# Optimization experiments

Hardware: AMD Instinct MI355X
Metric: run time of the kernel (lower is better)

The kernel has to match this reference:

```python
import jax, jax.numpy as jnp
import numpy as np

N_NODES = 100000
N_EDGES = 1600000
N_GRAPHS = 2048
DIM_IN, DIM_H, DIM_FC, DIM_OUT = 128, 128, 256, 8


def _glorot(key, shape):
    fan_in, fan_out = shape[0], shape[1]
    lim = float(np.sqrt(6.0 / (fan_in + fan_out)))
    return jax.random.uniform(key, shape, jnp.float32, -lim, lim)


def setup_inputs() -> dict:
    key = jax.random.key(0)
    ks = jax.random.split(key, 16)
    x = jax.random.normal(ks[0], (N_NODES, DIM_IN), jnp.float32)
    edge_index = jax.random.randint(ks[1], (2, N_EDGES), 0, N_NODES, jnp.int64)
    batch = jnp.sort(jax.random.randint(ks[2], (N_NODES,), 0, N_GRAPHS, jnp.int64))
    inp = {"x": x, "edge_index": edge_index, "batch": batch}
    # GraphConv layers: W_rel [in,out], W_root [in,out], b [out]
    dims = [(DIM_IN, DIM_H), (DIM_H, DIM_H), (DIM_H, DIM_H), (DIM_H, DIM_H)]
    for i, (di, do) in enumerate(dims, start=1):
        inp[f"W{i}_rel"] = _glorot(ks[2 + 3 * i], (di, do))
        inp[f"W{i}_root"] = _glorot(ks[3 + 3 * i], (di, do))
        inp[f"b{i}"] = jnp.zeros((do,), jnp.float32)
    inp["fc_w"] = _glorot(ks[3], (DIM_H, DIM_FC))
    inp["fc_b"] = jnp.zeros((DIM_FC,), jnp.float32)
    inp["reg_w"] = _glorot(ks[4], (DIM_FC, DIM_OUT))
    inp["reg_b"] = jnp.zeros((DIM_OUT,), jnp.float32)
    return inp


def _graph_conv(x, src, dst, w_rel, w_root, b):
    # PyG GraphConv (aggr='add'): out_i = W_rel @ sum_{j->i} x_j + W_root @ x_i + b
    agg = jax.ops.segment_sum(x[src], dst, num_segments=N_NODES)  # [N, d_in]
    return agg @ w_rel + x @ w_root + b


def reference(x, edge_index, batch,
              W1_rel, W1_root, b1, W2_rel, W2_root, b2,
              W3_rel, W3_root, b3, W4_rel, W4_root, b4,
              fc_w, fc_b, reg_w, reg_b):
    src, dst = edge_index[0], edge_index[1]
    h = jax.nn.relu(_graph_conv(x, src, dst, W1_rel, W1_root, b1))
    h = jax.nn.relu(_graph_conv(h, src, dst, W2_rel, W2_root, b2))
    h = jax.nn.relu(_graph_conv(h, src, dst, W3_rel, W3_root, b3))
    h = jax.nn.relu(_graph_conv(h, src, dst, W4_rel, W4_root, b4))
    # global_mean_pool over graphs
    sums = jax.ops.segment_sum(h, batch, num_segments=N_GRAPHS)  # [G, d]
    cnt = jax.ops.segment_sum(jnp.ones((h.shape[0],), h.dtype), batch,
                              num_segments=N_GRAPHS)
    pooled = sums / jnp.maximum(cnt, 1.0)[:, None]
    # dropout is identity at inference
    hfc = pooled @ fc_w + fc_b
    return hfc @ reg_w + reg_b  # [G, dim_out]
```

## Files before the change

### kernel.cpp

```cpp
#include <hip/hip_runtime.h>

#define N_NODES 100000
#define N_EDGES 1600000
#define N_GRAPHS 2048
#define DIM 128

#define NBUK 196
#define BUKSH 9
#define NCH 256
#define EPB 6250
#define NMAT (NBUK * NCH)

typedef short short8v __attribute__((ext_vector_type(8)));
typedef float float4v __attribute__((ext_vector_type(4)));

__device__ __forceinline__ unsigned short f2bf(float f) {
  union { float f; unsigned u; } x; x.f = f;
  unsigned r = x.u + 0x7fffu + ((x.u >> 16) & 1u);
  return (unsigned short)(r >> 16);
}
__device__ __forceinline__ float bfhi2f(unsigned bits) {
  union { unsigned u; float f; } x; x.u = bits; return x.f;
}
__device__ __forceinline__ void accum8(float* p, uint4 v) {
  p[0] += bfhi2f(v.x << 16); p[1] += bfhi2f(v.x & 0xffff0000u);
  p[2] += bfhi2f(v.y << 16); p[3] += bfhi2f(v.y & 0xffff0000u);
  p[4] += bfhi2f(v.z << 16); p[5] += bfhi2f(v.z & 0xffff0000u);
  p[6] += bfhi2f(v.w << 16); p[7] += bfhi2f(v.w & 0xffff0000u);
}

__global__ __launch_bounds__(256) void k_bcount(const int* __restrict__ dst, int* __restrict__ cntmat) {
  __shared__ int cnt[NBUK];
  int b = blockIdx.x, t = threadIdx.x;
  if (t < NBUK) cnt[t] = 0;
  __syncthreads();
  int e0 = b * EPB;
  for (int j = t; j < EPB; j += 256) atomicAdd(&cnt[dst[e0 + j] >> BUKSH], 1);
  __syncthreads();
  if (t < NBUK) cntmat[t * NCH + b] = cnt[t];
}

__global__ __launch_bounds__(256) void k_scan1g(const int* __restrict__ in, int n,
                                                int* __restrict__ tmp, int* __restrict__ bsum) {
  __shared__ int sh[256];
  int b = blockIdx.x, t = threadIdx.x;
  int base = b * 1024 + t * 4;
  int v[4], s = 0;
#pragma unroll
  for (int i = 0; i < 4; i++) { v[i] = (base + i < n) ? in[base + i] : 0; s += v[i]; }
  sh[t] = s;
  __syncthreads();
  for (int off = 1; off < 256; off <<= 1) {
    int x = (t >= off) ? sh[t - off] : 0;
    __syncthreads();
    sh[t] += x;
    __syncthreads();
  }
  int run = sh[t] - s;
#pragma unroll
  for (int i = 0; i < 4; i++) { run += v[i]; if (base + i < n) tmp[base + i] = run; }
  if (t == 255) bsum[b] = sh[255];
}

__global__ void k_scan2g(int* __restrict__ bsum, int nb) {
  __shared__ int sh[128];
  int t = threadIdx.x;
  int v = (t < nb) ? bsum[t] : 0;
  sh[t] = v;
  __syncthreads();
  for (int off = 1; off < 128; off <<= 1) {
    int x = (t >= off) ? sh[t - off] : 0;
    __syncthreads();
    sh[t] += x;
    __syncthreads();
  }
  if (t < nb) bsum[t] = sh[t] - v;
}

__global__ __launch_bounds__(256) void k_exc(const int* __restrict__ tmp, const int* __restrict__ bsum,
                                             const int* __restrict__ in, int n, int* __restrict__ outExc) {
  int i = blockIdx.x * 256 + threadIdx.x;
  if (i < n) outExc[i] = tmp[i] + bsum[i >> 10] - in[i];
}

__global__ __launch_bounds__(256) void k_bscatter(const int* __restrict__ src, const int* __restrict__ dst,
                                                  const int* __restrict__ base, int2* __restrict__ epk) {
  __shared__ int cur[NBUK];
  int b = blockIdx.x, t = threadIdx.x;
  if (t < NBUK) cur[t] = base[t * NCH + b];
  __syncthreads();
  int e0 = b * EPB;
  for (int j = t; j < EPB; j += 256) {
    int s = src[e0 + j], d = dst[e0 + j];
    int pos = atomicAdd(&cur[d >> BUKSH], 1);
    epk[pos] = make_int2(s, d);
  }
}

__global__ __launch_bounds__(256) void k_bfinish(const int2* __restrict__ epk, const int* __restrict__ base,
                                                 int* __restrict__ rowptr, int* __restrict__ col) {
  __shared__ int a[512];
  __shared__ int sh[256];
  int k = blockIdx.x, t = threadIdx.x;
  int bstart = base[k * NCH];
  int bend = (k + 1 < NBUK) ? base[(k + 1) * NCH] : N_EDGES;
  a[t] = 0; a[t + 256] = 0;
  __syncthreads();
  for (int i = bstart + t; i < bend; i += 256) atomicAdd(&a[epk[i].y - (k << BUKSH)], 1);
  __syncthreads();
  int c0 = a[2 * t], c1 = a[2 * t + 1];
  int s = c0 + c1;
  sh[t] = s;
  __syncthreads();
  for (int off = 1; off < 256; off <<= 1) {
    int x = (t >= off) ? sh[t - off] : 0;
    __syncthreads();
    sh[t] += x;
    __syncthreads();
  }
  int excl = sh[t] - s;
  int st0 = bstart + excl;
  int st1 = st0 + c0;
  int g0 = (k << BUKSH) + 2 * t, g1 = g0 + 1;
  if (g0 < N_NODES) rowptr[g0] = st0;
  if (g1 < N_NODES) rowptr[g1] = st1;
  if (k == NBUK - 1 && t == 0) rowptr[N_NODES] = N_EDGES;
  __syncthreads();
  a[2 * t] = st0; a[2 * t + 1] = st1;
  __syncthreads();
  for (int i = bstart + t; i < bend; i += 256) {
    int2 e = epk[i];
    int pos = atomicAdd(&a[e.y - (k << BUKSH)], 1);
    col[pos] = e.x;
  }
}

__global__ __launch_bounds__(256) void k_gptr(const int* __restrict__ batch, int* __restrict__ gptr) {
  int i = blockIdx.x * 256 + threadIdx.x;
  if (i >= N_NODES) return;
  int b = batch[i];
  int a = (i == 0) ? -1 : batch[i - 1];
  for (int g = a + 1; g <= b; g++) gptr[g] = i;
  if (i == N_NODES - 1) {
    for (int g = b + 1; g <= N_GRAPHS; g++) gptr[g] = N_NODES;
  }
}

__global__ __launch_bounds__(256) void k_cvtx(const float* __restrict__ x, unsigned short* __restrict__ h) {
  int i = blockIdx.x * 256 + threadIdx.x;
  if (i < N_NODES * DIM / 4) {
    float4 v = ((const float4*)x)[i];
    unsigned lo = (unsigned)f2bf(v.x) | ((unsigned)f2bf(v.y) << 16);
    unsigned hi = (unsigned)f2bf(v.z) | ((unsigned)f2bf(v.w) << 16);
    ((uint2*)h)[i] = make_uint2(lo, hi);
  }
}

__global__ __launch_bounds__(256) void k_cvtw(const float* w0, const float* w1, const float* w2, const float* w3,
                                              const float* w4, const float* w5, const float* w6, const float* w7,
                                              unsigned short* __restrict__ wbF) {
  int i = blockIdx.x * 256 + threadIdx.x;
  if (i < 4 * 8 * 8 * 64 * 8) {
    int j = i & 7, l = (i >> 3) & 63, c = (i >> 9) & 7, kc = (i >> 12) & 7, layer = i >> 15;
    int m = layer * 2 + (kc >> 2);
    const float* w;
    switch (m) {
      case 0: w = w0; break; case 1: w = w1; break; case 2: w = w2; break; case 3: w = w3; break;
      case 4: w = w4; break; case 5: w = w5; break; case 6: w = w6; break; default: w = w7; break;
    }
    int kin = (kc & 3) * 32 + ((l >> 4) * 8) + j;
    int n = c * 16 + (l & 15);
    wbF[i] = f2bf(w[kin * 128 + n]);
  }
}

__global__ __launch_bounds__(256, 8) void k_fused(const int* __restrict__ rowptr,
                                                  const int* __restrict__ col,
                                                  const unsigned short* __restrict__ hIn,
                                                  const unsigned short* __restrict__ wbF,
                                                  const float* __restrict__ bias,
                                                  unsigned short* __restrict__ hOut) {
  __shared__ uint4 As[1024];
  const int t = threadIdx.x;
  const int wave = t >> 6, lane = t & 63;
  const int wrow0 = blockIdx.x * 64 + wave * 16;
  const int sub = lane >> 4, li = lane & 15;

  for (int ri = 0; ri < 16; ri += 2) {
    int nodeA = wrow0 + ri;
    int nodeB = nodeA + 1;
    float pA[8], pB[8];
#pragma unroll
    for (int j = 0; j < 8; j++) { pA[j] = 0.f; pB[j] = 0.f; }
    int aS1 = 0, bS1 = 0, eA = 0, eB = 0;
    if (nodeA < N_NODES) { eA = rowptr[nodeA]; aS1 = rowptr[nodeA + 1]; }
    if (nodeB < N_NODES) { eB = rowptr[nodeB]; bS1 = rowptr[nodeB + 1]; }

    while (eA + 8 <= aS1 && eB + 8 <= bS1) {
      int cA0 = col[eA + sub], cA1 = col[eA + 4 + sub];
      int cB0 = col[eB + sub], cB1 = col[eB + 4 + sub];
      uint4 vA0 = *(const uint4*)(hIn + (size_t)cA0 * DIM + li * 8);
      uint4 vA1 = *(const uint4*)(hIn + (size_t)cA1 * DIM + li * 8);
      uint4 vB0 = *(const uint4*)(hIn + (size_t)cB0 * DIM + li * 8);
      uint4 vB1 = *(const uint4*)(hIn + (size_t)cB1 * DIM + li * 8);
      accum8(pA, vA0);
      accum8(pA, vA1);
      accum8(pB, vB0);
      accum8(pB, vB1);
      eA += 8; eB += 8;
    }
    for (; eA + 16 <= aS1; eA += 16) {
      int c0 = col[eA + sub], c1 = col[eA + 4 + sub], c2 = col[eA + 8 + sub], c3 = col[eA + 12 + sub];
      uint4 v0 = *(const uint4*)(hIn + (size_t)c0 * DIM + li * 8);
      uint4 v1 = *(const uint4*)(hIn + (size_t)c1 * DIM + li * 8);
      uint4 v2 = *(const uint4*)(hIn + (size_t)c2 * DIM + li * 8);
      uint4 v3 = *(const uint4*)(hIn + (size_t)c3 * DIM + li * 8);
      accum8(pA, v0); accum8(pA, v1); accum8(pA, v2); accum8(pA, v3);
    }
    if (eA + 8 <= aS1) {
      int c0 = col[eA + sub], c1 = col[eA + 4 + sub];
      uint4 v0 = *(const uint4*)(hIn + (size_t)c0 * DIM + li * 8);
      uint4 v1 = *(const uint4*)(hIn + (size_t)c1 * DIM + li * 8);
      accum8(pA, v0); accum8(pA, v1);
      eA += 8;
    }
    if (eA + 4 <= aS1) {
      int c0 = col[eA + sub];
      uint4 v0 = *(const uint4*)(hIn + (size_t)c0 * DIM + li * 8);
      accum8(pA, v0);
      eA += 4;
    }
    if (eA + sub < aS1) {
      int c0 = col[eA + sub];
      uint4 v0 = *(const uint4*)(hIn + (size_t)c0 * DIM + li * 8);
      accum8(pA, v0);
    }
    for (; eB + 16 <= bS1; eB += 16) {
      int c0 = col[eB + sub], c1 = col[eB + 4 + sub], c2 = col[eB + 8 + sub], c3 = col[eB + 12 + sub];
      uint4 v0 = *(const uint4*)(hIn + (size_t)c0 * DIM + li * 8);
      uint4 v1 = *(const uint4*)(hIn + (size_t)c1 * DIM + li * 8);
      uint4 v2 = *(const uint4*)(hIn + (size_t)c2 * DIM + li * 8);
      uint4 v3 = *(const uint4*)(hIn + (size_t)c3 * DIM + li * 8);
      accum8(pB, v0); accum8(pB, v1); accum8(pB, v2); accum8(pB, v3);
    }
    if (eB + 8 <= bS1) {
      int c0 = col[eB + sub], c1 = col[eB + 4 + sub];
      uint4 v0 = *(const uint4*)(hIn + (size_t)c0 * DIM + li * 8);
      uint4 v1 = *(const uint4*)(hIn + (size_t)c1 * DIM + li * 8);
      accum8(pB, v0); accum8(pB, v1);
      eB += 8;
    }
    if (eB + 4 <= bS1) {
      int c0 = col[eB + sub];
      uint4 v0 = *(const uint4*)(hIn + (size_t)c0 * DIM + li * 8);
      accum8(pB, v0);
      eB += 4;
    }
    if (eB + sub < bS1) {
      int c0 = col[eB + sub];
      uint4 v0 = *(const uint4*)(hIn + (size_t)c0 * DIM + li * 8);
      accum8(pB, v0);
    }

#pragma unroll
    for (int j = 0; j < 8; j++) {
      pA[j] += __shfl_xor(pA[j], 16, 64);
      pA[j] += __shfl_xor(pA[j], 32, 64);
      pB[j] += __shfl_xor(pB[j], 16, 64);
      pB[j] += __shfl_xor(pB[j], 32, 64);
    }
    if (sub == 0) {
      uint4 oA, oB;
      oA.x = (unsigned)f2bf(pA[0]) | ((unsigned)f2bf(pA[1]) << 16);
      oA.y = (unsigned)f2bf(pA[2]) | ((unsigned)f2bf(pA[3]) << 16);
      oA.z = (unsigned)f2bf(pA[4]) | ((unsigned)f2bf(pA[5]) << 16);
      oA.w = (unsigned)f2bf(pA[6]) | ((unsigned)f2bf(pA[7]) << 16);
      oB.x = (unsigned)f2bf(pB[0]) | ((unsigned)f2bf(pB[1]) << 16);
      oB.y = (unsigned)f2bf(pB[2]) | ((unsigned)f2bf(pB[3]) << 16);
      oB.z = (unsigned)f2bf(pB[4]) | ((unsigned)f2bf(pB[5]) << 16);
      oB.w = (unsigned)f2bf(pB[6]) | ((unsigned)f2bf(pB[7]) << 16);
      As[(wave * 16 + li) * 16 + (ri ^ li)] = oA;
      As[(wave * 16 + li) * 16 + ((ri + 1) ^ li)] = oB;
    }
  }

  float4v acc[8];
#pragma unroll
  for (int c2 = 0; c2 < 8; c2++)
#pragma unroll
    for (int i = 0; i < 4; i++) acc[c2][i] = 0.f;

#pragma unroll
  for (int kc = 0; kc < 4; kc++) {
    int c = kc * 4 + sub;
    short8v afr = *(const short8v*)&As[(wave * 16 + c) * 16 + (li ^ c)];
#pragma unroll
    for (int c2 = 0; c2 < 8; c2++) {
      short8v bfr = *(const short8v*)(wbF + (size_t)((kc * 8 + c2) * 64 + lane) * 8);
      acc[c2] = __builtin_amdgcn_mfma_f32_16x16x32_bf16(afr, bfr, acc[c2], 0, 0, 0);
    }
  }

#pragma unroll
  for (int j = 0; j < 4; j++) {
    int idx = j * 64 + lane;
    int r = idx >> 4, c = idx & 15;
    int rsrc = wrow0 + r; if (rsrc > N_NODES - 1) rsrc = N_NODES - 1;
    uint4 v = *(const uint4*)(hIn + (size_t)rsrc * DIM + c * 8);
    As[(wave * 16 + c) * 16 + (r ^ c)] = v;
  }

#pragma unroll
  for (int kc = 0; kc < 4; kc++) {
    int c = kc * 4 + sub;
    short8v afr = *(const short8v*)&As[(wave * 16 + c) * 16 + (li ^ c)];
#pragma unroll
    for (int c2 = 0; c2 < 8; c2++) {
      short8v bfr = *(const short8v*)(wbF + (size_t)(((4 + kc) * 8 + c2) * 64 + lane) * 8);
      acc[c2] = __builtin_amdgcn_mfma_f32_16x16x32_bf16(afr, bfr, acc[c2], 0, 0, 0);
    }
  }

  int rbase = wrow0 + sub * 4;
#pragma unroll
  for (int c2 = 0; c2 < 8; c2++) {
    int colidx = c2 * 16 + li;
    float bv = bias[colidx];
#pragma unroll
    for (int i = 0; i < 4; i++) {
      int row = rbase + i;
      if (row < N_NODES) {
        float v = acc[c2][i] + bv;
        v = v > 0.f ? v : 0.f;
        hOut[row * DIM + colidx] = f2bf(v);
      }
    }
  }
}

__global__ __launch_bounds__(256) void k_pool(const unsigned short* __restrict__ h,
                                              const int* __restrict__ gptr,
                                              float* __restrict__ pooledMean) {
  int g = blockIdx.x * 4 + (threadIdx.x >> 6);
  if (g >= N_GRAPHS) return;
  int lane = threadIdx.x & 63;
  int li = lane & 15;
  int s0 = gptr[g], s1 = gptr[g + 1];
  float p[8];
#pragma unroll
  for (int j = 0; j < 8; j++) p[j] = 0.f;
  int f1 = s1 * 16;
  for (int f = s0 * 16 + lane; f < f1; f += 64) {
    uint4 v = ((const uint4*)h)[f];
    accum8(p, v);
  }
#pragma unroll
  for (int j = 0; j < 8; j++) {
    p[j] += __shfl_xor(p[j], 16, 64);
    p[j] += __shfl_xor(p[j], 32, 64);
  }
  float inv = (s1 > s0) ? 1.f / (float)(s1 - s0) : 0.f;
  if (lane < 16) {
    float4 o0 = make_float4(p[0] * inv, p[1] * inv, p[2] * inv, p[3] * inv);
    float4 o1 = make_float4(p[4] * inv, p[5] * inv, p[6] * inv, p[7] * inv);
    *(float4*)(pooledMean + g * DIM + li * 8) = o0;
    *(float4*)(pooledMean + g * DIM + li * 8 + 4) = o1;
  }
}

__global__ __launch_bounds__(256) void k_fc(const float* __restrict__ pooledMean,
                                            const float* __restrict__ fc_w, const float* __restrict__ fc_b,
                                            const float* __restrict__ reg_w, const float* __restrict__ reg_b,
                                            float* __restrict__ out) {
  __shared__ float sp[128];
  __shared__ float shfc[256];
  __shared__ float red[64];
  int g = blockIdx.x, t = threadIdx.x;
  if (t < 128) sp[t] = pooledMean[g * DIM + t];
  __syncthreads();
  float a = fc_b[t];
  for (int k = 0; k < 128; k++) a += sp[k] * fc_w[k * 256 + t];
  shfc[t] = a;
  __syncthreads();
  if (t < 64) {
    int o = t & 7, seg = t >> 3;
    float r = 0.f;
    for (int j = seg * 32; j < seg * 32 + 32; j++) r += shfc[j] * reg_w[j * 8 + o];
    red[t] = r;
  }
  __syncthreads();
  if (t < 8) {
    float r = reg_b[t];
    for (int s = 0; s < 8; s++) r += red[s * 8 + t];
    out[g * 8 + t] = r;
  }
}

extern "C" void kernel_launch(void* const* d_in, const int* in_sizes, int n_in,
                              void* d_out, int out_size, void* d_ws, size_t ws_size,
                              hipStream_t stream) {
  (void)in_sizes; (void)n_in; (void)out_size; (void)ws_size;
  const float* x = (const float*)d_in[0];
  const int* ei = (const int*)d_in[1];
  const int* src = ei;
  const int* dst = ei + N_EDGES;
  const int* batch = (const int*)d_in[2];
  const float* Wrel[4]  = {(const float*)d_in[3], (const float*)d_in[6], (const float*)d_in[9],  (const float*)d_in[12]};
  const float* Wroot[4] = {(const float*)d_in[4], (const float*)d_in[7], (const float*)d_in[10], (const float*)d_in[13]};
  const float* bias[4]  = {(const float*)d_in[5], (const float*)d_in[8], (const float*)d_in[11], (const float*)d_in[14]};
  const float* fc_w  = (const float*)d_in[15];
  const float* fc_b  = (const float*)d_in[16];
  const float* reg_w = (const float*)d_in[17];
  const float* reg_b = (const float*)d_in[18];
  float* out = (float*)d_out;

  char* ws = (char*)d_ws;
  size_t off = 0;
  auto alloc = [&](size_t b) -> char* {
    char* p = ws + off;
    off = (off + b + 255) & ~(size_t)255;
    return p;
  };
  int* rowptr = (int*)alloc((N_NODES + 1) * 4);
  int* cntmat = (int*)alloc((size_t)NMAT * 4);
  int* tmpB   = (int*)alloc((size_t)NMAT * 4);
  int* bsumB  = (int*)alloc(128 * 4);
  int* base   = (int*)alloc((size_t)NMAT * 4);
  int2* epk   = (int2*)alloc((size_t)N_EDGES * 8);
  int* colws  = (int*)alloc((size_t)N_EDGES * 4);
  int* gptr   = (int*)alloc((N_GRAPHS + 1) * 4);
  unsigned short* wbF = (unsigned short*)alloc((size_t)4 * 32768 * 2);
  unsigned short* h_a = (unsigned short*)alloc((size_t)N_NODES * DIM * 2);
  unsigned short* h_b = (unsigned short*)alloc((size_t)N_NODES * DIM * 2);
  float* pooled = (float*)alloc((size_t)N_GRAPHS * DIM * 4);

  k_bcount<<<NCH, 256, 0, stream>>>(dst, cntmat);
  k_scan1g<<<NMAT / 1024, 256, 0, stream>>>(cntmat, NMAT, tmpB, bsumB);
  k_scan2g<<<1, 128, 0, stream>>>(bsumB, NMAT / 1024);
  k_exc<<<(NMAT + 255) / 256, 256, 0, stream>>>(tmpB, bsumB, cntmat, NMAT, base);
  k_bscatter<<<NCH, 256, 0, stream>>>(src, dst, base, epk);
  k_bfinish<<<NBUK, 256, 0, stream>>>(epk, base, rowptr, colws);

  k_gptr<<<(N_NODES + 255) / 256, 256, 0, stream>>>(batch, gptr);
  k_cvtx<<<(N_NODES * DIM / 4 + 255) / 256, 256, 0, stream>>>(x, h_a);
  k_cvtw<<<(4 * 32768 + 255) / 256, 256, 0, stream>>>(
      Wrel[0], Wroot[0], Wrel[1], Wroot[1], Wrel[2], Wroot[2], Wrel[3], Wroot[3], wbF);

  unsigned short* h_in = h_a;
  unsigned short* h_out = h_b;
  const int FB = (N_NODES + 63) / 64;
  for (int l = 0; l < 4; l++) {
    k_fused<<<FB, 256, 0, stream>>>(rowptr, colws, h_in, wbF + (size_t)l * 32768, bias[l], h_out);
    unsigned short* t2 = h_in; h_in = h_out; h_out = t2;
  }

  k_pool<<<(N_GRAPHS + 3) / 4, 256, 0, stream>>>(h_in, gptr, pooled);
  k_fc<<<N_GRAPHS, 256, 0, stream>>>(pooled, fc_w, fc_b, reg_w, reg_b, out);
}
```

Baseline: 506.3 us.

## Stage per-wave column indices in LDS and software-pipeline gather loads

Each wave now preloads the column indices for its 16 nodes into shared memory when they fit in a fixed budget, so gathers take indices from LDS instead of dependent global loads. The paired-node loop is software-pipelined, issuing the next row loads before accumulating the current ones. Blocks shrink from 256 to 128 threads with 32 nodes per block and new launch bounds. The node bounds checks on rowptr reads were removed, which relies on the rowptr layout for tail nodes. Registers rise from the pipelined loads and occupancy changes.

After: 598.6 us. 18.2% more time.

```diff
diff --git a/kernel.cpp b/kernel.cpp
--- a/kernel.cpp
+++ b/kernel.cpp
@@ -10,6 +10,8 @@
 #define NCH 256
 #define EPB 6250
 #define NMAT (NBUK * NCH)
+
+#define CB 512
 
 typedef short short8v __attribute__((ext_vector_type(8)));
 typedef float float4v __attribute__((ext_vector_type(4)));
@@ -174,91 +176,85 @@
   }
 }
 
-__global__ __launch_bounds__(256, 8) void k_fused(const int* __restrict__ rowptr,
-                                                  const int* __restrict__ col,
-                                                  const unsigned short* __restrict__ hIn,
-                                                  const unsigned short* __restrict__ wbF,
-                                                  const float* __restrict__ bias,
-                                                  unsigned short* __restrict__ hOut) {
-  __shared__ uint4 As[1024];
-  const int t = threadIdx.x;
-  const int wave = t >> 6, lane = t & 63;
-  const int wrow0 = blockIdx.x * 64 + wave * 16;
-  const int sub = lane >> 4, li = lane & 15;
-
+template<bool LC>
+__device__ __forceinline__ void gnn_phase1(const int* __restrict__ rowptr,
+                                           const int* __restrict__ col,
+                                           const int* cbuf, int e0,
+                                           const unsigned short* __restrict__ hIn,
+                                           uint4* Asl, int wrow0, int sub, int li) {
+#define GCOL(e) (LC ? cbuf[(e) - e0] : col[(e)])
+#define ROWLD(c) (*(const uint4*)(hIn + (size_t)(c) * DIM + li * 8))
   for (int ri = 0; ri < 16; ri += 2) {
-    int nodeA = wrow0 + ri;
-    int nodeB = nodeA + 1;
+    const int nodeA = wrow0 + ri;
     float pA[8], pB[8];
 #pragma unroll
     for (int j = 0; j < 8; j++) { pA[j] = 0.f; pB[j] = 0.f; }
-    int aS1 = 0, bS1 = 0, eA = 0, eB = 0;
-    if (nodeA < N_NODES) { eA = rowptr[nodeA]; aS1 = rowptr[nodeA + 1]; }
-    if (nodeB < N_NODES) { eB = rowptr[nodeB]; bS1 = rowptr[nodeB + 1]; }
-
-    while (eA + 8 <= aS1 && eB + 8 <= bS1) {
-      int cA0 = col[eA + sub], cA1 = col[eA + 4 + sub];
-      int cB0 = col[eB + sub], cB1 = col[eB + 4 + sub];
-      uint4 vA0 = *(const uint4*)(hIn + (size_t)cA0 * DIM + li * 8);
-      uint4 vA1 = *(const uint4*)(hIn + (size_t)cA1 * DIM + li * 8);
-      uint4 vB0 = *(const uint4*)(hIn + (size_t)cB0 * DIM + li * 8);
-      uint4 vB1 = *(const uint4*)(hIn + (size_t)cB1 * DIM + li * 8);
-      accum8(pA, vA0);
-      accum8(pA, vA1);
-      accum8(pB, vB0);
-      accum8(pB, vB1);
+    int eA = rowptr[nodeA];
+    int aS1 = rowptr[nodeA + 1];
+    int eB = aS1;
+    int bS1 = rowptr[nodeA + 2];
+
+    if (eA + 8 <= aS1 && eB + 8 <= bS1) {
+      int cA0 = GCOL(eA + sub), cA1 = GCOL(eA + 4 + sub);
+      int cB0 = GCOL(eB + sub), cB1 = GCOL(eB + 4 + sub);
+      uint4 vA0 = ROWLD(cA0), vA1 = ROWLD(cA1);
+      uint4 vB0 = ROWLD(cB0), vB1 = ROWLD(cB1);
       eA += 8; eB += 8;
+      while (eA + 8 <= aS1 && eB + 8 <= bS1) {
+        int nA0 = GCOL(eA + sub), nA1 = GCOL(eA + 4 + sub);
+        int nB0 = GCOL(eB + sub), nB1 = GCOL(eB + 4 + sub);
+        uint4 wA0 = ROWLD(nA0), wA1 = ROWLD(nA1);
+        uint4 wB0 = ROWLD(nB0), wB1 = ROWLD(nB1);
+        accum8(pA, vA0); accum8(pA, vA1);
+        accum8(pB, vB0); accum8(pB, vB1);
+        vA0 = wA0; vA1 = wA1; vB0 = wB0; vB1 = wB1;
+        eA += 8; eB += 8;
+      }
+      accum8(pA, vA0); accum8(pA, vA1);
+      accum8(pB, vB0); accum8(pB, vB1);
     }
     for (; eA + 16 <= aS1; eA += 16) {
-      int c0 = col[eA + sub], c1 = col[eA + 4 + sub], c2 = col[eA + 8 + sub], c3 = col[eA + 12 + sub];
-      uint4 v0 = *(const uint4*)(hIn + (size_t)c0 * DIM + li * 8);
-      uint4 v1 = *(const uint4*)(hIn + (size_t)c1 * DIM + li * 8);
-      uint4 v2 = *(const uint4*)(hIn + (size_t)c2 * DIM + li * 8);
-      uint4 v3 = *(const uint4*)(hIn + (size_t)c3 * DIM + li * 8);
+      int c0 = GCOL(eA + sub), c1 = GCOL(eA + 4 + sub), c2 = GCOL(eA + 8 + sub), c3 = GCOL(eA + 12 + sub);
+      uint4 v0 = ROWLD(c0), v1 = ROWLD(c1), v2 = ROWLD(c2), v3 = ROWLD(c3);
       accum8(pA, v0); accum8(pA, v1); accum8(pA, v2); accum8(pA, v3);
     }
     if (eA + 8 <= aS1) {
-      int c0 = col[eA + sub], c1 = col[eA + 4 + sub];
-      uint4 v0 = *(const uint4*)(hIn + (size_t)c0 * DIM + li * 8);
-      uint4 v1 = *(const uint4*)(hIn + (size_t)c1 * DIM + li * 8);
+      int c0 = GCOL(eA + sub), c1 = GCOL(eA + 4 + sub);
+      uint4 v0 = ROWLD(c0), v1 = ROWLD(c1);
       accum8(pA, v0); accum8(pA, v1);
       eA += 8;
     }
     if (eA + 4 <= aS1) {
-      int c0 = col[eA + sub];
-      uint4 v0 = *(const uint4*)(hIn + (size_t)c0 * DIM + li * 8);
+      int c0 = GCOL(eA + sub);
+      uint4 v0 = ROWLD(c0);
       accum8(pA, v0);
       eA += 4;
     }
     if (eA + sub < aS1) {
-      int c0 = col[eA + sub];
-      uint4 v0 = *(const uint4*)(hIn + (size_t)c0 * DIM + li * 8);
+      int c0 = GCOL(eA + sub);
+      uint4 v0 = ROWLD(c0);
       accum8(pA, v0);
     }
     for (; eB + 16 <= bS1; eB += 16) {
-      int c0 = col[eB + sub], c1 = col[eB + 4 + sub], c2 = col[eB + 8 + sub], c3 = col[eB + 12 + sub];
-      uint4 v0 = *(const uint4*)(hIn + (size_t)c0 * DIM + li * 8);
-      uint4 v1 = *(const uint4*)(hIn + (size_t)c1 * DIM + li * 8);
-      uint4 v2 = *(const uint4*)(hIn + (size_t)c2 * DIM + li * 8);
-      uint4 v3 = *(const uint4*)(hIn + (size_t)c3 * DIM + li * 8);
+      int c0 = GCOL(eB + sub), c1 = GCOL(eB + 4 + sub), c2 = GCOL(eB + 8 + sub), c3 = GCOL(eB + 12 + sub);
+      uint4 v0 = ROWLD(c0), v1 = ROWLD(c1), v2 = ROWLD(c2), v3 = ROWLD(c3);
       accum8(pB, v0); accum8(pB, v1); accum8(pB, v2); accum8(pB, v3);
     }
     if (eB + 8 <= bS1) {
-      int c0 = col[eB + sub], c1 = col[eB + 4 + sub];
-      uint4 v0 = *(const uint4*)(hIn + (size_t)c0 * DIM + li * 8);
-      uint4 v1 = *(const uint4*)(hIn + (size_t)c1 * DIM + li * 8);
+      int c0 = GCOL(eB + sub), c1 = GCOL(eB + 4 + sub);
+      uint4 v0 = ROWLD(c0), v1 = ROWLD(c1);
       accum8(pB, v0); accum8(pB, v1);
       eB += 8;
     }
     if (eB + 4 <= bS1) {
-      int c0 = col[eB + sub];
-      uint4 v0 = *(const uint4*)(hIn + (size_t)c0 * DIM + li * 8);
+      int c0 = GCOL(eB + sub);
+      uint4 v0 = ROWLD(c0);
       accum8(pB, v0);
       eB += 4;
     }
     if (eB + sub < bS1) {
-      int c0 = col[eB + sub];
-      uint4 v0 = *(const uint4*)(hIn + (size_t)c0 * DIM + li * 8);
+      int c0 = GCOL(eB + sub);
+      uint4 v0 = ROWLD(c0);
       accum8(pB, v0);
     }
 
@@ -279,10 +275,39 @@
       oB.y = (unsigned)f2bf(pB[2]) | ((unsigned)f2bf(pB[3]) << 16);
       oB.z = (unsigned)f2bf(pB[4]) | ((unsigned)f2bf(pB[5]) << 16);
       oB.w = (unsigned)f2bf(pB[6]) | ((unsigned)f2bf(pB[7]) << 16);
-      As[(wave * 16 + li) * 16 + (ri ^ li)] = oA;
-      As[(wave * 16 + li) * 16 + ((ri + 1) ^ li)] = oB;
-    }
-  }
+      Asl[li * 16 + (ri ^ li)] = oA;
+      Asl[li * 16 + ((ri + 1) ^ li)] = oB;
+    }
+  }
+#undef GCOL
+#undef ROWLD
+}
+
+__global__ __launch_bounds__(128, 6) void k_fused(const int* __restrict__ rowptr,
+                                                  const int* __restrict__ col,
+                                                  const unsigned short* __restrict__ hIn,
+                                                  const unsigned short* __restrict__ wbF,
+                                                  const float* __restrict__ bias,
+                                                  unsigned short* __restrict__ hOut) {
+  __shared__ uint4 As[512];
+  __shared__ int colsh[2 * CB];
+  const int t = threadIdx.x;
+  const int wave = t >> 6, lane = t & 63;
+  const int wrow0 = blockIdx.x * 32 + wave * 16;
+  const int sub = lane >> 4, li = lane & 15;
+
+  const int e0 = rowptr[wrow0];
+  const int e1 = rowptr[wrow0 + 16];
+  const int ecnt = e1 - e0;
+  int* cbuf = &colsh[wave * CB];
+  const bool useLds = (ecnt <= CB);
+  if (useLds) {
+    for (int i = lane; i < ecnt; i += 64) cbuf[i] = col[e0 + i];
+  }
+  uint4* Asl = &As[wave * 256];
+
+  if (useLds) gnn_phase1<true>(rowptr, col, cbuf, e0, hIn, Asl, wrow0, sub, li);
+  else        gnn_phase1<false>(rowptr, col, cbuf, e0, hIn, Asl, wrow0, sub, li);
 
   float4v acc[8];
 #pragma unroll
@@ -293,7 +318,7 @@
 #pragma unroll
   for (int kc = 0; kc < 4; kc++) {
     int c = kc * 4 + sub;
-    short8v afr = *(const short8v*)&As[(wave * 16 + c) * 16 + (li ^ c)];
+    short8v afr = *(const short8v*)&Asl[c * 16 + (li ^ c)];
 #pragma unroll
     for (int c2 = 0; c2 < 8; c2++) {
       short8v bfr = *(const short8v*)(wbF + (size_t)((kc * 8 + c2) * 64 + lane) * 8);
@@ -307,13 +332,13 @@
     int r = idx >> 4, c = idx & 15;
     int rsrc = wrow0 + r; if (rsrc > N_NODES - 1) rsrc = N_NODES - 1;
     uint4 v = *(const uint4*)(hIn + (size_t)rsrc * DIM + c * 8);
-    As[(wave * 16 + c) * 16 + (r ^ c)] = v;
+    Asl[c * 16 + (r ^ c)] = v;
   }
 
 #pragma unroll
   for (int kc = 0; kc < 4; kc++) {
     int c = kc * 4 + sub;
-    short8v afr = *(const short8v*)&As[(wave * 16 + c) * 16 + (li ^ c)];
+    short8v afr = *(const short8v*)&Asl[c * 16 + (li ^ c)];
 #pragma unroll
     for (int c2 = 0; c2 < 8; c2++) {
       short8v bfr = *(const short8v*)(wbF + (size_t)(((4 + kc) * 8 + c2) * 64 + lane) * 8);
@@ -448,9 +473,9 @@
 
   unsigned short* h_in = h_a;
   unsigned short* h_out = h_b;
-  const int FB = (N_NODES + 63) / 64;
+  const int FB = (N_NODES + 31) / 32;
   for (int l = 0; l < 4; l++) {
-    k_fused<<<FB, 256, 0, stream>>>(rowptr, colws, h_in, wbF + (size_t)l * 32768, bias[l], h_out);
+    k_fused<<<FB, 128, 0, stream>>>(rowptr, colws, h_in, wbF + (size_t)l * 32768, bias[l], h_out);
     unsigned short* t2 = h_in; h_in = h_out; h_out = t2;
   }
 
```

## Gather four nodes at once with prefetched column indices and sched barriers

Applied to the files above, without the earlier changes.

The fused gather-plus-MFMA kernel now processes four destination nodes per iteration instead of two. Column indices for the next iteration are prefetched while the current row loads are in flight. Sched barriers keep all loads issued ahead of the accumulation. The occupancy hint drops from 8 to 5 blocks to make room for the larger register footprint, trading latency hiding across waves for more memory-level parallelism within each wave.

Result: slower. 772.7 us (+52.6%).

```diff
diff --git a/kernel.cpp b/kernel.cpp
--- a/kernel.cpp
+++ b/kernel.cpp
@@ -13,6 +13,8 @@
 
 typedef short short8v __attribute__((ext_vector_type(8)));
 typedef float float4v __attribute__((ext_vector_type(4)));
+
+#define SB() __builtin_amdgcn_sched_barrier(0)
 
 __device__ __forceinline__ unsigned short f2bf(float f) {
   union { float f; unsigned u; } x; x.f = f;
@@ -174,7 +176,78 @@
   }
 }
 
-__global__ __launch_bounds__(256, 8) void k_fused(const int* __restrict__ rowptr,
+#define ROWLD(c) (*(const uint4*)(hIn + (size_t)(c) * DIM + li * 8))
+
+__device__ __forceinline__ void pair_gather(const int* __restrict__ col,
+                                            const unsigned short* __restrict__ hIn,
+                                            int sub, int li,
+                                            int eA, int aS1, int eB, int bS1,
+                                            float* pA, float* pB) {
+  while (eA + 8 <= aS1 && eB + 8 <= bS1) {
+    int cA0 = col[eA + sub], cA1 = col[eA + 4 + sub];
+    int cB0 = col[eB + sub], cB1 = col[eB + 4 + sub];
+    uint4 vA0 = ROWLD(cA0);
+    uint4 vA1 = ROWLD(cA1);
+    uint4 vB0 = ROWLD(cB0);
+    uint4 vB1 = ROWLD(cB1);
+    SB();
+    accum8(pA, vA0);
+    accum8(pA, vA1);
+    accum8(pB, vB0);
+    accum8(pB, vB1);
+    eA += 8; eB += 8;
+  }
+  for (; eA + 16 <= aS1; eA += 16) {
+    int c0 = col[eA + sub], c1 = col[eA + 4 + sub], c2 = col[eA + 8 + sub], c3 = col[eA + 12 + sub];
+    uint4 v0 = ROWLD(c0), v1 = ROWLD(c1), v2 = ROWLD(c2), v3 = ROWLD(c3);
+    SB();
+    accum8(pA, v0); accum8(pA, v1); accum8(pA, v2); accum8(pA, v3);
+  }
+  if (eA + 8 <= aS1) {
+    int c0 = col[eA + sub], c1 = col[eA + 4 + sub];
+    uint4 v0 = ROWLD(c0), v1 = ROWLD(c1);
+    SB();
+    accum8(pA, v0); accum8(pA, v1);
+    eA += 8;
+  }
+  if (eA + 4 <= aS1) {
+    int c0 = col[eA + sub];
+    uint4 v0 = ROWLD(c0);
+    accum8(pA, v0);
+    eA += 4;
+  }
+  if (eA + sub < aS1) {
+    int c0 = col[eA + sub];
+    uint4 v0 = ROWLD(c0);
+    accum8(pA, v0);
+  }
+  for (; eB + 16 <= bS1; eB += 16) {
+    int c0 = col[eB + sub], c1 = col[eB + 4 + sub], c2 = col[eB + 8 + sub], c3 = col[eB + 12 + sub];
+    uint4 v0 = ROWLD(c0), v1 = ROWLD(c1), v2 = ROWLD(c2), v3 = ROWLD(c3);
+    SB();
+    accum8(pB, v0); accum8(pB, v1); accum8(pB, v2); accum8(pB, v3);
+  }
+  if (eB + 8 <= bS1) {
+    int c0 = col[eB + sub], c1 = col[eB + 4 + sub];
+    uint4 v0 = ROWLD(c0), v1 = ROWLD(c1);
+    SB();
+    accum8(pB, v0); accum8(pB, v1);
+    eB += 8;
+  }
+  if (eB + 4 <= bS1) {
+    int c0 = col[eB + sub];
+    uint4 v0 = ROWLD(c0);
+    accum8(pB, v0);
+    eB += 4;
+  }
+  if (eB + sub < bS1) {
+    int c0 = col[eB + sub];
+    uint4 v0 = ROWLD(c0);
+    accum8(pB, v0);
+  }
+}
+
+__global__ __launch_bounds__(256, 5) void k_fused(const int* __restrict__ rowptr,
                                                   const int* __restrict__ col,
                                                   const unsigned short* __restrict__ hIn,
                                                   const unsigned short* __restrict__ wbF,
@@ -186,101 +259,79 @@
   const int wrow0 = blockIdx.x * 64 + wave * 16;
   const int sub = lane >> 4, li = lane & 15;
 
-  for (int ri = 0; ri < 16; ri += 2) {
-    int nodeA = wrow0 + ri;
-    int nodeB = nodeA + 1;
-    float pA[8], pB[8];
-#pragma unroll
-    for (int j = 0; j < 8; j++) { pA[j] = 0.f; pB[j] = 0.f; }
-    int aS1 = 0, bS1 = 0, eA = 0, eB = 0;
-    if (nodeA < N_NODES) { eA = rowptr[nodeA]; aS1 = rowptr[nodeA + 1]; }
-    if (nodeB < N_NODES) { eB = rowptr[nodeB]; bS1 = rowptr[nodeB + 1]; }
-
-    while (eA + 8 <= aS1 && eB + 8 <= bS1) {
-      int cA0 = col[eA + sub], cA1 = col[eA + 4 + sub];
-      int cB0 = col[eB + sub], cB1 = col[eB + 4 + sub];
-      uint4 vA0 = *(const uint4*)(hIn + (size_t)cA0 * DIM + li * 8);
-      uint4 vA1 = *(const uint4*)(hIn + (size_t)cA1 * DIM + li * 8);
-      uint4 vB0 = *(const uint4*)(hIn + (size_t)cB0 * DIM + li * 8);
-      uint4 vB1 = *(const uint4*)(hIn + (size_t)cB1 * DIM + li * 8);
-      accum8(pA, vA0);
-      accum8(pA, vA1);
-      accum8(pB, vB0);
-      accum8(pB, vB1);
-      eA += 8; eB += 8;
-    }
-    for (; eA + 16 <= aS1; eA += 16) {
-      int c0 = col[eA + sub], c1 = col[eA + 4 + sub], c2 = col[eA + 8 + sub], c3 = col[eA + 12 + sub];
-      uint4 v0 = *(const uint4*)(hIn + (size_t)c0 * DIM + li * 8);
-      uint4 v1 = *(const uint4*)(hIn + (size_t)c1 * DIM + li * 8);
-      uint4 v2 = *(const uint4*)(hIn + (size_t)c2 * DIM + li * 8);
-      uint4 v3 = *(const uint4*)(hIn + (size_t)c3 * DIM + li * 8);
-      accum8(pA, v0); accum8(pA, v1); accum8(pA, v2); accum8(pA, v3);
-    }
-    if (eA + 8 <= aS1) {
-      int c0 = col[eA + sub], c1 = col[eA + 4 + sub];
-      uint4 v0 = *(const uint4*)(hIn + (size_t)c0 * DIM + li * 8);
-      uint4 v1 = *(const uint4*)(hIn + (size_t)c1 * DIM + li * 8);
-      accum8(pA, v0); accum8(pA, v1);
-      eA += 8;
-    }
-    if (eA + 4 <= aS1) {
-      int c0 = col[eA + sub];
-      uint4 v0 = *(const uint4*)(hIn + (size_t)c0 * DIM + li * 8);
-      accum8(pA, v0);
-      eA += 4;
-    }
-    if (eA + sub < aS1) {
-      int c0 = col[eA + sub];
-      uint4 v0 = *(const uint4*)(hIn + (size_t)c0 * DIM + li * 8);
-      accum8(pA, v0);
-    }
-    for (; eB + 16 <= bS1; eB += 16) {
-      int c0 = col[eB + sub], c1 = col[eB + 4 + sub], c2 = col[eB + 8 + sub], c3 = col[eB + 12 + sub];
-      uint4 v0 = *(const uint4*)(hIn + (size_t)c0 * DIM + li * 8);
-      uint4 v1 = *(const uint4*)(hIn + (size_t)c1 * DIM + li * 8);
-      uint4 v2 = *(const uint4*)(hIn + (size_t)c2 * DIM + li * 8);
-      uint4 v3 = *(const uint4*)(hIn + (size_t)c3 * DIM + li * 8);
-      accum8(pB, v0); accum8(pB, v1); accum8(pB, v2); accum8(pB, v3);
-    }
-    if (eB + 8 <= bS1) {
-      int c0 = col[eB + sub], c1 = col[eB + 4 + sub];
-      uint4 v0 = *(const uint4*)(hIn + (size_t)c0 * DIM + li * 8);
-      uint4 v1 = *(const uint4*)(hIn + (size_t)c1 * DIM + li * 8);
-      accum8(pB, v0); accum8(pB, v1);
-      eB += 8;
-    }
-    if (eB + 4 <= bS1) {
-      int c0 = col[eB + sub];
-      uint4 v0 = *(const uint4*)(hIn + (size_t)c0 * DIM + li * 8);
-      accum8(pB, v0);
-      eB += 4;
-    }
-    if (eB + sub < bS1) {
-      int c0 = col[eB + sub];
-      uint4 v0 = *(const uint4*)(hIn + (size_t)c0 * DIM + li * 8);
-      accum8(pB, v0);
-    }
+  for (int ri = 0; ri < 16; ri += 4) {
+    const int n0 = wrow0 + ri;
+    float p0[8], p1[8], p2[8], p3[8];
+#pragma unroll
+    for (int j = 0; j < 8; j++) { p0[j] = 0.f; p1[j] = 0.f; p2[j] = 0.f; p3[j] = 0.f; }
+    int e0 = 0, s0 = 0, e1 = 0, s1 = 0, e2 = 0, s2 = 0, e3 = 0, s3 = 0;
+    if (n0     < N_NODES) { e0 = rowptr[n0];     s0 = rowptr[n0 + 1]; }
+    if (n0 + 1 < N_NODES) { e1 = rowptr[n0 + 1]; s1 = rowptr[n0 + 2]; }
+    if (n0 + 2 < N_NODES) { e2 = rowptr[n0 + 2]; s2 = rowptr[n0 + 3]; }
+    if (n0 + 3 < N_NODES) { e3 = rowptr[n0 + 3]; s3 = rowptr[n0 + 4]; }
+
+    bool go = (e0 + 8 <= s0) && (e1 + 8 <= s1) && (e2 + 8 <= s2) && (e3 + 8 <= s3);
+    int c00, c01, c10, c11, c20, c21, c30, c31;
+    if (go) {
+      c00 = col[e0 + sub]; c01 = col[e0 + 4 + sub];
+      c10 = col[e1 + sub]; c11 = col[e1 + 4 + sub];
+      c20 = col[e2 + sub]; c21 = col[e2 + 4 + sub];
+      c30 = col[e3 + sub]; c31 = col[e3 + 4 + sub];
+    }
+    while (go) {
+      uint4 v00 = ROWLD(c00), v01 = ROWLD(c01);
+      uint4 v10 = ROWLD(c10), v11 = ROWLD(c11);
+      uint4 v20 = ROWLD(c20), v21 = ROWLD(c21);
+      uint4 v30 = ROWLD(c30), v31 = ROWLD(c31);
+      e0 += 8; e1 += 8; e2 += 8; e3 += 8;
+      go = (e0 + 8 <= s0) && (e1 + 8 <= s1) && (e2 + 8 <= s2) && (e3 + 8 <= s3);
+      int f0 = go ? e0 : 0, f1 = go ? e1 : 0, f2 = go ? e2 : 0, f3 = go ? e3 : 0;
+      c00 = col[f0 + sub]; c01 = col[f0 + 4 + sub];
+      c10 = col[f1 + sub]; c11 = col[f1 + 4 + sub];
+      c20 = col[f2 + sub]; c21 = col[f2 + 4 + sub];
+      c30 = col[f3 + sub]; c31 = col[f3 + 4 + sub];
+      SB();
+      accum8(p0, v00); accum8(p0, v01);
+      accum8(p1, v10); accum8(p1, v11);
+      accum8(p2, v20); accum8(p2, v21);
+      accum8(p3, v30); accum8(p3, v31);
+    }
+    pair_gather(col, hIn, sub, li, e0, s0, e1, s1, p0, p1);
+    pair_gather(col, hIn, sub, li, e2, s2, e3, s3, p2, p3);
 
 #pragma unroll
     for (int j = 0; j < 8; j++) {
-      pA[j] += __shfl_xor(pA[j], 16, 64);
-      pA[j] += __shfl_xor(pA[j], 32, 64);
-      pB[j] += __shfl_xor(pB[j], 16, 64);
-      pB[j] += __shfl_xor(pB[j], 32, 64);
+      p0[j] += __shfl_xor(p0[j], 16, 64);
+      p0[j] += __shfl_xor(p0[j], 32, 64);
+      p1[j] += __shfl_xor(p1[j], 16, 64);
+      p1[j] += __shfl_xor(p1[j], 32, 64);
+      p2[j] += __shfl_xor(p2[j], 16, 64);
+      p2[j] += __shfl_xor(p2[j], 32, 64);
+      p3[j] += __shfl_xor(p3[j], 16, 64);
+      p3[j] += __shfl_xor(p3[j], 32, 64);
     }
     if (sub == 0) {
-      uint4 oA, oB;
-      oA.x = (unsigned)f2bf(pA[0]) | ((unsigned)f2bf(pA[1]) << 16);
-      oA.y = (unsigned)f2bf(pA[2]) | ((unsigned)f2bf(pA[3]) << 16);
-      oA.z = (unsigned)f2bf(pA[4]) | ((unsigned)f2bf(pA[5]) << 16);
-      oA.w = (unsigned)f2bf(pA[6]) | ((unsigned)f2bf(pA[7]) << 16);
-      oB.x = (unsigned)f2bf(pB[0]) | ((unsigned)f2bf(pB[1]) << 16);
-      oB.y = (unsigned)f2bf(pB[2]) | ((unsigned)f2bf(pB[3]) << 16);
-      oB.z = (unsigned)f2bf(pB[4]) | ((unsigned)f2bf(pB[5]) << 16);
-      oB.w = (unsigned)f2bf(pB[6]) | ((unsigned)f2bf(pB[7]) << 16);
-      As[(wave * 16 + li) * 16 + (ri ^ li)] = oA;
-      As[(wave * 16 + li) * 16 + ((ri + 1) ^ li)] = oB;
+      uint4 o0, o1, o2, o3;
+      o0.x = (unsigned)f2bf(p0[0]) | ((unsigned)f2bf(p0[1]) << 16);
+      o0.y = (unsigned)f2bf(p0[2]) | ((unsigned)f2bf(p0[3]) << 16);
+      o0.z = (unsigned)f2bf(p0[4]) | ((unsigned)f2bf(p0[5]) << 16);
+      o0.w = (unsigned)f2bf(p0[6]) | ((unsigned)f2bf(p0[7]) << 16);
+      o1.x = (unsigned)f2bf(p1[0]) | ((unsigned)f2bf(p1[1]) << 16);
+      o1.y = (unsigned)f2bf(p1[2]) | ((unsigned)f2bf(p1[3]) << 16);
+      o1.z = (unsigned)f2bf(p1[4]) | ((unsigned)f2bf(p1[5]) << 16);
+      o1.w = (unsigned)f2bf(p1[6]) | ((unsigned)f2bf(p1[7]) << 16);
+      o2.x = (unsigned)f2bf(p2[0]) | ((unsigned)f2bf(p2[1]) << 16);
+      o2.y = (unsigned)f2bf(p2[2]) | ((unsigned)f2bf(p2[3]) << 16);
+      o2.z = (unsigned)f2bf(p2[4]) | ((unsigned)f2bf(p2[5]) << 16);
+      o2.w = (unsigned)f2bf(p2[6]) | ((unsigned)f2bf(p2[7]) << 16);
+      o3.x = (unsigned)f2bf(p3[0]) | ((unsigned)f2bf(p3[1]) << 16);
+      o3.y = (unsigned)f2bf(p3[2]) | ((unsigned)f2bf(p3[3]) << 16);
+      o3.z = (unsigned)f2bf(p3[4]) | ((unsigned)f2bf(p3[5]) << 16);
+      o3.w = (unsigned)f2bf(p3[6]) | ((unsigned)f2bf(p3[7]) << 16);
+      As[(wave * 16 + li) * 16 + ((ri)     ^ li)] = o0;
+      As[(wave * 16 + li) * 16 + ((ri + 1) ^ li)] = o1;
+      As[(wave * 16 + li) * 16 + ((ri + 2) ^ li)] = o2;
+      As[(wave * 16 + li) * 16 + ((ri + 3) ^ li)] = o3;
     }
   }
 
```

## Gather one node per 16-lane group with prefetched column indices

Applied to the files above, without the earlier changes.

Reworks the fused aggregation so each 16-lane quarter of a wave handles its own node, with four nodes per iteration instead of two nodes spread across all four quarters. The cross-lane shuffle reduction goes away. Column indices for the next 8-edge chunk are software-prefetched before the current chunk is accumulated, with a sched_barrier to hold that ordering. Occupancy hint drops from 8 to 6 blocks per CU to fit the extra registers. The risk is more divergence from uneven node degrees within a wave, and lower occupancy.

Measured after the change: 754.5 us. 49.0% more time.

```diff
diff --git a/kernel.cpp b/kernel.cpp
--- a/kernel.cpp
+++ b/kernel.cpp
@@ -13,6 +13,9 @@
 
 typedef short short8v __attribute__((ext_vector_type(8)));
 typedef float float4v __attribute__((ext_vector_type(4)));
+typedef float float8v __attribute__((ext_vector_type(8)));
+
+#define SB() __builtin_amdgcn_sched_barrier(0)
 
 __device__ __forceinline__ unsigned short f2bf(float f) {
   union { float f; unsigned u; } x; x.f = f;
@@ -21,6 +24,12 @@
 }
 __device__ __forceinline__ float bfhi2f(unsigned bits) {
   union { unsigned u; float f; } x; x.u = bits; return x.f;
+}
+__device__ __forceinline__ void acc8v(float8v& p, uint4 v) {
+  p[0] += bfhi2f(v.x << 16); p[1] += bfhi2f(v.x & 0xffff0000u);
+  p[2] += bfhi2f(v.y << 16); p[3] += bfhi2f(v.y & 0xffff0000u);
+  p[4] += bfhi2f(v.z << 16); p[5] += bfhi2f(v.z & 0xffff0000u);
+  p[6] += bfhi2f(v.w << 16); p[7] += bfhi2f(v.w & 0xffff0000u);
 }
 __device__ __forceinline__ void accum8(float* p, uint4 v) {
   p[0] += bfhi2f(v.x << 16); p[1] += bfhi2f(v.x & 0xffff0000u);
@@ -174,7 +183,9 @@
   }
 }
 
-__global__ __launch_bounds__(256, 8) void k_fused(const int* __restrict__ rowptr,
+#define ROWLD(c) (*(const uint4*)(hIn + (size_t)(c) * DIM + li * 8))
+
+__global__ __launch_bounds__(256, 6) void k_fused(const int* __restrict__ rowptr,
                                                   const int* __restrict__ col,
                                                   const unsigned short* __restrict__ hIn,
                                                   const unsigned short* __restrict__ wbF,
@@ -186,102 +197,52 @@
   const int wrow0 = blockIdx.x * 64 + wave * 16;
   const int sub = lane >> 4, li = lane & 15;
 
-  for (int ri = 0; ri < 16; ri += 2) {
-    int nodeA = wrow0 + ri;
-    int nodeB = nodeA + 1;
-    float pA[8], pB[8];
-#pragma unroll
-    for (int j = 0; j < 8; j++) { pA[j] = 0.f; pB[j] = 0.f; }
-    int aS1 = 0, bS1 = 0, eA = 0, eB = 0;
-    if (nodeA < N_NODES) { eA = rowptr[nodeA]; aS1 = rowptr[nodeA + 1]; }
-    if (nodeB < N_NODES) { eB = rowptr[nodeB]; bS1 = rowptr[nodeB + 1]; }
-
-    while (eA + 8 <= aS1 && eB + 8 <= bS1) {
-      int cA0 = col[eA + sub], cA1 = col[eA + 4 + sub];
-      int cB0 = col[eB + sub], cB1 = col[eB + 4 + sub];
-      uint4 vA0 = *(const uint4*)(hIn + (size_t)cA0 * DIM + li * 8);
-      uint4 vA1 = *(const uint4*)(hIn + (size_t)cA1 * DIM + li * 8);
-      uint4 vB0 = *(const uint4*)(hIn + (size_t)cB0 * DIM + li * 8);
-      uint4 vB1 = *(const uint4*)(hIn + (size_t)cB1 * DIM + li * 8);
-      accum8(pA, vA0);
-      accum8(pA, vA1);
-      accum8(pB, vB0);
-      accum8(pB, vB1);
-      eA += 8; eB += 8;
-    }
-    for (; eA + 16 <= aS1; eA += 16) {
-      int c0 = col[eA + sub], c1 = col[eA + 4 + sub], c2 = col[eA + 8 + sub], c3 = col[eA + 12 + sub];
-      uint4 v0 = *(const uint4*)(hIn + (size_t)c0 * DIM + li * 8);
-      uint4 v1 = *(const uint4*)(hIn + (size_t)c1 * DIM + li * 8);
-      uint4 v2 = *(const uint4*)(hIn + (size_t)c2 * DIM + li * 8);
-      uint4 v3 = *(const uint4*)(hIn + (size_t)c3 * DIM + li * 8);
-      accum8(pA, v0); accum8(pA, v1); accum8(pA, v2); accum8(pA, v3);
-    }
-    if (eA + 8 <= aS1) {
-      int c0 = col[eA + sub], c1 = col[eA + 4 + sub];
-      uint4 v0 = *(const uint4*)(hIn + (size_t)c0 * DIM + li * 8);
-      uint4 v1 = *(const uint4*)(hIn + (size_t)c1 * DIM + li * 8);
-      accum8(pA, v0); accum8(pA, v1);
-      eA += 8;
-    }
-    if (eA + 4 <= aS1) {
-      int c0 = col[eA + sub];
-      uint4 v0 = *(const uint4*)(hIn + (size_t)c0 * DIM + li * 8);
-      accum8(pA, v0);
-      eA += 4;
-    }
-    if (eA + sub < aS1) {
-      int c0 = col[eA + sub];
-      uint4 v0 = *(const uint4*)(hIn + (size_t)c0 * DIM + li * 8);
-      accum8(pA, v0);
-    }
-    for (; eB + 16 <= bS1; eB += 16) {
-      int c0 = col[eB + sub], c1 = col[eB + 4 + sub], c2 = col[eB + 8 + sub], c3 = col[eB + 12 + sub];
-      uint4 v0 = *(const uint4*)(hIn + (size_t)c0 * DIM + li * 8);
-      uint4 v1 = *(const uint4*)(hIn + (size_t)c1 * DIM + li * 8);
-      uint4 v2 = *(const uint4*)(hIn + (size_t)c2 * DIM + li * 8);
-      uint4 v3 = *(const uint4*)(hIn + (size_t)c3 * DIM + li * 8);
-      accum8(pB, v0); accum8(pB, v1); accum8(pB, v2); accum8(pB, v3);
-    }
-    if (eB + 8 <= bS1) {
-      int c0 = col[eB + sub], c1 = col[eB + 4 + sub];
-      uint4 v0 = *(const uint4*)(hIn + (size_t)c0 * DIM + li * 8);
-      uint4 v1 = *(const uint4*)(hIn + (size_t)c1 * DIM + li * 8);
-      accum8(pB, v0); accum8(pB, v1);
-      eB += 8;
-    }
-    if (eB + 4 <= bS1) {
-      int c0 = col[eB + sub];
-      uint4 v0 = *(const uint4*)(hIn + (size_t)c0 * DIM + li * 8);
-      accum8(pB, v0);
-      eB += 4;
-    }
-    if (eB + sub < bS1) {
-      int c0 = col[eB + sub];
-      uint4 v0 = *(const uint4*)(hIn + (size_t)c0 * DIM + li * 8);
-      accum8(pB, v0);
-    }
-
-#pragma unroll
-    for (int j = 0; j < 8; j++) {
-      pA[j] += __shfl_xor(pA[j], 16, 64);
-      pA[j] += __shfl_xor(pA[j], 32, 64);
-      pB[j] += __shfl_xor(pB[j], 16, 64);
-      pB[j] += __shfl_xor(pB[j], 32, 64);
-    }
-    if (sub == 0) {
-      uint4 oA, oB;
-      oA.x = (unsigned)f2bf(pA[0]) | ((unsigned)f2bf(pA[1]) << 16);
-      oA.y = (unsigned)f2bf(pA[2]) | ((unsigned)f2bf(pA[3]) << 16);
-      oA.z = (unsigned)f2bf(pA[4]) | ((unsigned)f2bf(pA[5]) << 16);
-      oA.w = (unsigned)f2bf(pA[6]) | ((unsigned)f2bf(pA[7]) << 16);
-      oB.x = (unsigned)f2bf(pB[0]) | ((unsigned)f2bf(pB[1]) << 16);
-      oB.y = (unsigned)f2bf(pB[2]) | ((unsigned)f2bf(pB[3]) << 16);
-      oB.z = (unsigned)f2bf(pB[4]) | ((unsigned)f2bf(pB[5]) << 16);
-      oB.w = (unsigned)f2bf(pB[6]) | ((unsigned)f2bf(pB[7]) << 16);
-      As[(wave * 16 + li) * 16 + (ri ^ li)] = oA;
-      As[(wave * 16 + li) * 16 + ((ri + 1) ^ li)] = oB;
-    }
+  for (int ri = 0; ri < 16; ri += 4) {
+    const int r = wrow0 + ri + sub;
+    int e = 0, end = 0;
+    if (r < N_NODES) { e = rowptr[r]; end = rowptr[r + 1]; }
+    float8v p = {0.f, 0.f, 0.f, 0.f, 0.f, 0.f, 0.f, 0.f};
+
+    int c0, c1, c2, c3, c4, c5, c6, c7;
+    bool go = (e + 8 <= end);
+    if (go) {
+      c0 = col[e];     c1 = col[e + 1]; c2 = col[e + 2]; c3 = col[e + 3];
+      c4 = col[e + 4]; c5 = col[e + 5]; c6 = col[e + 6]; c7 = col[e + 7];
+    }
+    while (go) {
+      uint4 v0 = ROWLD(c0), v1 = ROWLD(c1), v2 = ROWLD(c2), v3 = ROWLD(c3);
+      uint4 v4 = ROWLD(c4), v5 = ROWLD(c5), v6 = ROWLD(c6), v7 = ROWLD(c7);
+      e += 8;
+      go = (e + 8 <= end);
+      int f = go ? e : 0;
+      c0 = col[f];     c1 = col[f + 1]; c2 = col[f + 2]; c3 = col[f + 3];
+      c4 = col[f + 4]; c5 = col[f + 5]; c6 = col[f + 6]; c7 = col[f + 7];
+      SB();
+      acc8v(p, v0); acc8v(p, v1); acc8v(p, v2); acc8v(p, v3);
+      acc8v(p, v4); acc8v(p, v5); acc8v(p, v6); acc8v(p, v7);
+    }
+    if (e + 4 <= end) {
+      int d0 = col[e], d1 = col[e + 1], d2 = col[e + 2], d3 = col[e + 3];
+      uint4 v0 = ROWLD(d0), v1 = ROWLD(d1), v2 = ROWLD(d2), v3 = ROWLD(d3);
+      acc8v(p, v0); acc8v(p, v1); acc8v(p, v2); acc8v(p, v3);
+      e += 4;
+    }
+    {
+      int rem = end - e;
+      int t0 = (rem > 0) ? col[e] : 0;
+      int t1 = (rem > 1) ? col[e + 1] : 0;
+      int t2 = (rem > 2) ? col[e + 2] : 0;
+      uint4 w0 = ROWLD(t0), w1 = ROWLD(t1), w2 = ROWLD(t2);
+      if (rem > 0) acc8v(p, w0);
+      if (rem > 1) acc8v(p, w1);
+      if (rem > 2) acc8v(p, w2);
+    }
+    uint4 o;
+    o.x = (unsigned)f2bf(p[0]) | ((unsigned)f2bf(p[1]) << 16);
+    o.y = (unsigned)f2bf(p[2]) | ((unsigned)f2bf(p[3]) << 16);
+    o.z = (unsigned)f2bf(p[4]) | ((unsigned)f2bf(p[5]) << 16);
+    o.w = (unsigned)f2bf(p[6]) | ((unsigned)f2bf(p[7]) << 16);
+    As[(wave * 16 + li) * 16 + ((ri + sub) ^ li)] = o;
   }
 
   float4v acc[8];
```
